# Performance work log

Hardware: AMD Instinct MI355X
Metric: run time of the kernel (lower is better)

The kernel has to match this reference:

```python
import jax, jax.numpy as jnp
import numpy as np

B, N, D, H = 2, 2048, 512, 8
HD = D // H
EPS = 1e-5


def layernorm(x, g, b):
    m = jnp.mean(x, axis=-1, keepdims=True)
    v = jnp.var(x, axis=-1, keepdims=True)
    return (x - m) * jax.lax.rsqrt(v + EPS) * g + b


def setup_inputs() -> dict:
    key = jax.random.key(0)
    ks = jax.random.split(key, 16)
    s = 1.0 / np.sqrt(D)
    def lin(k, din, dout):
        k1, k2 = jax.random.split(k)
        return (jax.random.uniform(k1, (din, dout), jnp.float32, -s, s),
                jax.random.uniform(k2, (dout,), jnp.float32, -s, s))
    Wq, bq = lin(ks[0], D, D)
    Wk, bk = lin(ks[1], D, D)
    Wv, bv = lin(ks[2], D, D)
    Wo, bo = lin(ks[3], D, D)
    W1, b1 = lin(ks[4], D, 2 * D)
    W2, b2 = lin(ks[5], 2 * D, D)
    return {
        'y': jax.random.normal(ks[6], (B, N, D), jnp.float32),
        'Wq': Wq, 'bq': bq, 'Wk': Wk, 'bk': bk, 'Wv': Wv, 'bv': bv,
        'Wo': Wo, 'bo': bo,
        'ln1_g': jnp.ones((D,)), 'ln1_b': jnp.zeros((D,)),
        'ln2_g': jnp.ones((D,)), 'ln2_b': jnp.zeros((D,)),
        'W1': W1, 'b1': b1, 'W2': W2, 'b2': b2,
    }


def reference(y, Wq, bq, Wk, bk, Wv, bv, Wo, bo, ln1_g, ln1_b, ln2_g, ln2_b, W1, b1, W2, b2):
    x = layernorm(y, ln1_g, ln1_b)
    def heads(W, b):
        return (x @ W + b).reshape(B, N, H, HD).transpose(0, 2, 1, 3)  # bhnc
    q = heads(Wq, bq)
    k = heads(Wk, bk)
    v = heads(Wv, bv)
    score = jax.nn.softmax(jnp.einsum('bhic,bhjc->bhij', q, k) / np.sqrt(HD), axis=-1)
    r = jnp.einsum('bhij,bhjc->bhic', score, v)
    r = r.transpose(0, 2, 1, 3).reshape(B, N, D) @ Wo + bo
    y = y + r
    h = layernorm(y, ln2_g, ln2_b)
    h = jax.nn.gelu(h @ W1 + b1, approximate=False) @ W2 + b2
    return y + h
```

## Files before the change

### kernel.cpp

```cpp
#include <hip/hip_runtime.h>

#define DEVI __device__ __forceinline__

typedef unsigned short u16;
typedef unsigned int   u32;
typedef unsigned long long u64;
typedef float  f32x4  __attribute__((ext_vector_type(4)));
typedef __bf16 bf16x8 __attribute__((ext_vector_type(8)));

union FragU { bf16x8 b; u64 u[2]; __bf16 e[8]; };

DEVI u16 f2b(float x) { __bf16 t = (__bf16)x; return __builtin_bit_cast(u16, t); }

DEVI float exp2a(float x) { float r; asm("v_exp_f32 %0, %1" : "=v"(r) : "v"(x)); return r; }

DEVI void gload16(const void* g, void* l) {
  __builtin_amdgcn_global_load_lds((const __attribute__((address_space(1))) u32*)g,
                                   (__attribute__((address_space(3))) u32*)l, 16, 0, 0);
}

DEVI int kperm(int b) {
  return (b & 0x47) | ((b & 0x18) << 1) | ((b & 0x20) >> 2);
}
DEVI int swzo(int row, int b) {
  const int p = kperm(b);
  return ((((p >> 4) ^ row) & 7) << 4) | (p & 15);
}
DEVI FragU ldfrag(const char* base, int row, int g) {
  return *reinterpret_cast<const FragU*>(base + row * 128 + (((g ^ (row & 7)) << 4)));
}
DEVI size_t gaddr(int row, int kbyte, int rowbytes) {
  return (size_t)row * rowbytes + (size_t)((kbyte & ~127) + swzo(row, kbyte & 127));
}

__global__ __launch_bounds__(256)
void prep(const float* __restrict__ Wq, const float* __restrict__ Wk,
          const float* __restrict__ Wv, const float* __restrict__ Wo,
          const float* __restrict__ W1, const float* __restrict__ W2,
          u16* __restrict__ wqkvT, u16* __restrict__ woT,
          u16* __restrict__ w1T, u16* __restrict__ w2T,
          const float* __restrict__ y, const float* __restrict__ ln1g,
          const float* __restrict__ ln1b, char* __restrict__ xb) {
  const int id = blockIdx.x;
  if (id < 2048) {
    __shared__ float tile[32][33];
    const float* src; u16* dst; int K, N, bx, by;
    if (id < 1024) {
      const int m = id >> 8, t = id & 255;
      K = 512; N = 512; bx = t & 15; by = t >> 4;
      src = (m == 0) ? Wq : (m == 1) ? Wk : (m == 2) ? Wv : Wo;
      dst = (m == 3) ? woT : wqkvT + m * 512 * 512;
    } else if (id < 1536) {
      const int t = id - 1024; K = 512; N = 1024; bx = t & 31; by = t >> 5;
      src = W1; dst = w1T;
    } else {
      const int t = id - 1536; K = 1024; N = 512; bx = t & 15; by = t >> 4;
      src = W2; dst = w2T;
    }
    const int tx = threadIdx.x & 31, ty = threadIdx.x >> 5;
#pragma unroll
    for (int i = 0; i < 4; ++i)
      tile[ty + i * 8][tx] = src[(size_t)(by * 32 + ty + i * 8) * N + bx * 32 + tx];
    __syncthreads();
    const int nl = threadIdx.x >> 3, kq = threadIdx.x & 7;
    const int n = bx * 32 + nl;
    const int kg = by * 32 + kq * 4;
    union { ushort4 s; u64 q; } pk;
    pk.s.x = f2b(tile[kq * 4 + 0][nl]);
    pk.s.y = f2b(tile[kq * 4 + 1][nl]);
    pk.s.z = f2b(tile[kq * 4 + 2][nl]);
    pk.s.w = f2b(tile[kq * 4 + 3][nl]);
    *(u64*)((char*)dst + gaddr(n, 2 * kg, 2 * K)) = pk.q;
  } else {
    const int row = id - 2048;
    const int t = threadIdx.x;
    const float2 v = ((const float2*)(y + (size_t)row * 512))[t];
    float s1 = v.x + v.y, s2 = v.x * v.x + v.y * v.y;
#pragma unroll
    for (int off = 32; off; off >>= 1) { s1 += __shfl_xor(s1, off); s2 += __shfl_xor(s2, off); }
    __shared__ float a1[4], a2[4];
    const int w = t >> 6;
    if ((t & 63) == 0) { a1[w] = s1; a2[w] = s2; }
    __syncthreads();
    s1 = a1[0] + a1[1] + a1[2] + a1[3];
    s2 = a2[0] + a2[1] + a2[2] + a2[3];
    const float mean = s1 * (1.f / 512.f);
    const float var = s2 * (1.f / 512.f) - mean * mean;
    const float rstd = rsqrtf(var + 1e-5f);
    const float2 gg = ((const float2*)ln1g)[t];
    const float2 bb = ((const float2*)ln1b)[t];
    const u16 o0 = f2b((v.x - mean) * rstd * gg.x + bb.x);
    const u16 o1 = f2b((v.y - mean) * rstd * gg.y + bb.y);
    *(u32*)(xb + gaddr(row, 4 * t, 1024)) = (u32)o0 | ((u32)o1 << 16);
  }
}

__global__ __launch_bounds__(256)
void ln_bf16(const float* __restrict__ x, const float* __restrict__ g,
             const float* __restrict__ b, char* __restrict__ out) {
  const int row = blockIdx.x;
  const int t = threadIdx.x;
  const float2 v = ((const float2*)(x + (size_t)row * 512))[t];
  float s1 = v.x + v.y, s2 = v.x * v.x + v.y * v.y;
#pragma unroll
  for (int off = 32; off; off >>= 1) { s1 += __shfl_xor(s1, off); s2 += __shfl_xor(s2, off); }
  __shared__ float a1[4], a2[4];
  const int w = t >> 6;
  if ((t & 63) == 0) { a1[w] = s1; a2[w] = s2; }
  __syncthreads();
  s1 = a1[0] + a1[1] + a1[2] + a1[3];
  s2 = a2[0] + a2[1] + a2[2] + a2[3];
  const float mean = s1 * (1.f / 512.f);
  const float var = s2 * (1.f / 512.f) - mean * mean;
  const float rstd = rsqrtf(var + 1e-5f);
  const float2 gg = ((const float2*)g)[t];
  const float2 bb = ((const float2*)b)[t];
  const u16 o0 = f2b((v.x - mean) * rstd * gg.x + bb.x);
  const u16 o1 = f2b((v.y - mean) * rstd * gg.y + bb.y);
  *(u32*)(out + gaddr(row, 4 * t, 1024)) = (u32)o0 | ((u32)o1 << 16);
}

enum { EPI_QKV = 0, EPI_RES = 1, EPI_GELU = 2 };

template <int EPI, int WM, int WN, int AM, int AN>
__global__ __launch_bounds__(WM * WN * 64)
void gemm_bf16(const char* __restrict__ A, const char* __restrict__ Bt, int N, int K,
               const float* __restrict__ bias,
               const float* __restrict__ bq, const float* __restrict__ bk,
               const float* __restrict__ bv,
               const float* __restrict__ res, float* __restrict__ outF,
               char* __restrict__ outB,
               u16* __restrict__ qo, char* __restrict__ ko, char* __restrict__ vo) {
  constexpr int NW = WM * WN;
  constexpr int TM = WM * AM * 16, TN = WN * AN * 16;
  constexpr int NCHA = TM / 8, NCHB = TN / 8, NCH = NCHA + NCHB;
  constexpr int CPW = NCH / NW;
  static_assert(CPW * NW == NCH, "chunk split");
  __shared__ __align__(16) char sA[2][TM * 128];
  __shared__ __align__(16) char sB[2][TN * 128];
  const int tid = threadIdx.x;
  const int l = tid & 63, w = tid >> 6;
  const int tm = blockIdx.x, tn = blockIdx.y;
  const int wr = w / WN, wc = w % WN;
  const int u = l >> 4, r16 = l & 15;
  const int lrow = l >> 3, lgr = l & 7;
  f32x4 acc[AM][AN] = {};
  const size_t KB = (size_t)K * 2;
  const char* Ab = A + (size_t)(tm * TM) * KB;
  const char* Bb = Bt + (size_t)(tn * TN) * KB;
  const int nkt = K >> 6;
  auto stage = [&](int buf, int kt) {
#pragma unroll
    for (int i = 0; i < CPW; ++i) {
      const int c = w * CPW + i;
      if (c < NCHA) {
        gload16(Ab + (size_t)(c * 8 + lrow) * KB + (size_t)kt * 128 + (lgr << 4),
                sA[buf] + c * 1024);
      } else {
        const int c2 = c - NCHA;
        gload16(Bb + (size_t)(c2 * 8 + lrow) * KB + (size_t)kt * 128 + (lgr << 4),
                sB[buf] + c2 * 1024);
      }
    }
  };
  stage(0, 0);
  int cur = 0;
  for (int kt = 0; kt < nkt; ++kt) {
    __syncthreads();
    if (kt + 1 < nkt) stage(cur ^ 1, kt + 1);
    __builtin_amdgcn_s_setprio(1);
#pragma unroll
    for (int ks = 0; ks < 2; ++ks) {
      FragU af[AM], bfr[AN];
      const int g = ks * 4 + u;
#pragma unroll
      for (int i = 0; i < AM; ++i)
        af[i] = ldfrag(sA[cur], wr * (AM * 16) + i * 16 + r16, g);
#pragma unroll
      for (int i = 0; i < AN; ++i)
        bfr[i] = ldfrag(sB[cur], wc * (AN * 16) + i * 16 + r16, g);
#pragma unroll
      for (int mi = 0; mi < AM; ++mi)
#pragma unroll
        for (int ni = 0; ni < AN; ++ni)
          acc[mi][ni] = __builtin_amdgcn_mfma_f32_16x16x32_bf16(af[mi].b, bfr[ni].b,
                                                                acc[mi][ni], 0, 0, 0);
    }
    __builtin_amdgcn_s_setprio(0);
    cur ^= 1;
  }
  const int row0 = tm * TM + wr * (AM * 16) + (u << 2);
  const int col0 = tn * TN + wc * (AN * 16) + r16;
#pragma unroll
  for (int mi = 0; mi < AM; ++mi) {
#pragma unroll
    for (int ni = 0; ni < AN; ++ni) {
      const int col = col0 + ni * 16;
      if (EPI == EPI_RES) {
#pragma unroll
        for (int r = 0; r < 4; ++r) {
          const int row = row0 + mi * 16 + r;
          outF[(size_t)row * N + col] = acc[mi][ni][r] + bias[col] + res[(size_t)row * N + col];
        }
      } else if (EPI == EPI_GELU) {
#pragma unroll
        for (int r = 0; r < 4; ++r) {
          const int row = row0 + mi * 16 + r;
          const float x = acc[mi][ni][r] + bias[col];
          *(u16*)(outB + gaddr(row, 2 * col, 2 * N)) =
              f2b(0.5f * x * (1.f + erff(x * 0.70710678118f)));
        }
      } else {
        const int which = col >> 9, cc = col & 511;
        const int h = cc >> 6, hd = cc & 63;
        if (which == 2) {
          const int rowa = row0 + mi * 16;
          const int bb2 = rowa >> 11, nt0 = rowa & 2047;
          const int bh = bb2 * 8 + h;
          const float bvv = bv[cc];
          union { ushort4 s; u64 q; } pk;
          pk.s.x = f2b(acc[mi][ni][0] + bvv);
          pk.s.y = f2b(acc[mi][ni][1] + bvv);
          pk.s.z = f2b(acc[mi][ni][2] + bvv);
          pk.s.w = f2b(acc[mi][ni][3] + bvv);
          *(u64*)(vo + (size_t)bh * 262144 + (size_t)(nt0 >> 6) * 8192 +
                  gaddr(hd, 2 * (nt0 & 63), 128)) = pk.q;
        } else {
#pragma unroll
          for (int r = 0; r < 4; ++r) {
            const int row = row0 + mi * 16 + r;
            const int bb2 = row >> 11, nt = row & 2047;
            const int bh = bb2 * 8 + h;
            if (which == 0)
              qo[((size_t)bh * 2048 + nt) * 64 + hd] = f2b((acc[mi][ni][r] + bq[cc]) * 0.18033688f);
            else
              *(u16*)(ko + (size_t)bh * 262144 + (size_t)(nt >> 6) * 8192 +
                      gaddr(nt & 63, 2 * hd, 128)) = f2b(acc[mi][ni][r] + bk[cc]);
          }
        }
      }
    }
  }
}

__global__ __launch_bounds__(512)
void attn_k(const u16* __restrict__ q, const char* __restrict__ kswz,
            const char* __restrict__ vswz, char* __restrict__ r_out) {
  __shared__ __align__(16) char sK[2][2][8192];
  __shared__ __align__(16) char sV[2][2][8192];
  const int tid = threadIdx.x;
  const int l = tid & 63, w = tid >> 6;
  const int kvh = w & 1, qw = w >> 1;
  const int bh = blockIdx.x, qt = blockIdx.y;
  const int u = l >> 4, r16 = l & 15;
  const char* kp = kswz + (size_t)bh * 262144;
  const char* vp = vswz + (size_t)bh * 262144;
  const int c0 = qw * 2;
  auto stage = [&](int buf, int t) {
#pragma unroll
    for (int c = 0; c < 2; ++c) {
      gload16(kp + (size_t)t * 8192 + (c0 + c) * 1024 + l * 16, sK[kvh][buf] + (c0 + c) * 1024);
      gload16(vp + (size_t)t * 8192 + (c0 + c) * 1024 + l * 16, sV[kvh][buf] + (c0 + c) * 1024);
    }
  };
  stage(0, kvh * 16);
  FragU qf[2], ones;
  {
    const u16* qr = q + (size_t)bh * (2048 * 64) + (size_t)(qt * 64 + qw * 16 + r16) * 64 + (u << 2);
    qf[0].u[0] = *(const u64*)qr;        qf[0].u[1] = *(const u64*)(qr + 16);
    qf[1].u[0] = *(const u64*)(qr + 32); qf[1].u[1] = *(const u64*)(qr + 48);
    ones.u[0] = 0x3F803F803F803F80ull;
    ones.u[1] = 0x3F803F803F803F80ull;
  }
  f32x4 o[4] = {};
  f32x4 lacc = {};
  int cur = 0;
  for (int i = 0; i < 16; ++i) {
    __syncthreads();
    if (i < 15) stage(cur ^ 1, kvh * 16 + i + 1);
    f32x4 st[4] = {};
    __builtin_amdgcn_s_setprio(1);
#pragma unroll
    for (int ks = 0; ks < 2; ++ks) {
      const int g = ks * 4 + u;
#pragma unroll
      for (int mi = 0; mi < 4; ++mi) {
        const FragU kf = ldfrag(sK[kvh][cur], mi * 16 + r16, g);
        st[mi] = __builtin_amdgcn_mfma_f32_16x16x32_bf16(kf.b, qf[ks].b, st[mi], 0, 0, 0);
      }
    }
    __builtin_amdgcn_s_setprio(0);
#pragma unroll
    for (int mi = 0; mi < 4; ++mi)
#pragma unroll
      for (int r = 0; r < 4; ++r) st[mi][r] = exp2a(st[mi][r]);
    FragU pb[2];
#pragma unroll
    for (int ks = 0; ks < 2; ++ks)
#pragma unroll
      for (int j = 0; j < 4; ++j) {
        pb[ks].e[j]     = (__bf16)st[2 * ks][j];
        pb[ks].e[j + 4] = (__bf16)st[2 * ks + 1][j];
      }
    __builtin_amdgcn_s_setprio(1);
#pragma unroll
    for (int ks = 0; ks < 2; ++ks) {
      const int g = ks * 4 + u;
      lacc = __builtin_amdgcn_mfma_f32_16x16x32_bf16(ones.b, pb[ks].b, lacc, 0, 0, 0);
#pragma unroll
      for (int mo = 0; mo < 4; ++mo) {
        const FragU vf = ldfrag(sV[kvh][cur], mo * 16 + r16, g);
        o[mo] = __builtin_amdgcn_mfma_f32_16x16x32_bf16(vf.b, pb[ks].b, o[mo], 0, 0, 0);
      }
    }
    __builtin_amdgcn_s_setprio(0);
    cur ^= 1;
  }
  __syncthreads();
  float* scrO = (float*)&sK[0][0][0];
  float* scrL = (float*)&sV[0][0][0];
  if (kvh == 1) {
    if (u == 0) scrL[qw * 32 + r16] = lacc[0];
#pragma unroll
    for (int mo = 0; mo < 4; ++mo)
#pragma unroll
      for (int r = 0; r < 4; ++r)
        scrO[qw * 1024 + (mo * 16 + u * 4 + r) * 16 + r16] = o[mo][r];
  }
  __syncthreads();
  if (kvh == 0) {
    const float linv = 1.f / (lacc[0] + scrL[qw * 32 + r16]);
    const int tok = (bh >> 3) * 2048 + qt * 64 + qw * 16 + r16;
    const int h = bh & 7;
#pragma unroll
    for (int mo = 0; mo < 4; ++mo) {
      union { ushort4 s; u64 qq; } pk;
      float vv[4];
#pragma unroll
      for (int r = 0; r < 4; ++r)
        vv[r] = (o[mo][r] + scrO[qw * 1024 + (mo * 16 + u * 4 + r) * 16 + r16]) * linv;
      pk.s.x = f2b(vv[0]); pk.s.y = f2b(vv[1]); pk.s.z = f2b(vv[2]); pk.s.w = f2b(vv[3]);
      *(u64*)(r_out + (size_t)tok * 1024 + h * 128 + swzo(tok, mo * 32 + (u << 3))) = pk.qq;
    }
  }
}

extern "C" void kernel_launch(void* const* d_in, const int* in_sizes, int n_in,
                              void* d_out, int out_size, void* d_ws, size_t ws_size,
                              hipStream_t stream) {
  const float* y    = (const float*)d_in[0];
  const float* Wq   = (const float*)d_in[1];
  const float* bq   = (const float*)d_in[2];
  const float* Wk   = (const float*)d_in[3];
  const float* bk   = (const float*)d_in[4];
  const float* Wv   = (const float*)d_in[5];
  const float* bv   = (const float*)d_in[6];
  const float* Wo   = (const float*)d_in[7];
  const float* bo   = (const float*)d_in[8];
  const float* ln1g = (const float*)d_in[9];
  const float* ln1b = (const float*)d_in[10];
  const float* ln2g = (const float*)d_in[11];
  const float* ln2b = (const float*)d_in[12];
  const float* W1   = (const float*)d_in[13];
  const float* b1   = (const float*)d_in[14];
  const float* W2   = (const float*)d_in[15];
  const float* b2   = (const float*)d_in[16];
  float* out = (float*)d_out;
  char* ws = (char*)d_ws;
  char* xb    = ws;
  u16*  qb    = (u16*)(ws + (4u << 20));
  char* kswz  = ws + (8u << 20);
  char* vswz  = ws + (12u << 20);
  char* rb    = ws + (16u << 20);
  char* g1b   = ws + (20u << 20);
  u16* wqkvT  = (u16*)(ws + (28u << 20));
  u16* woT    = wqkvT + 1536 * 512;
  u16* w1T    = woT + 512 * 512;
  u16* w2T    = w1T + 1024 * 512;

  prep<<<6144, 256, 0, stream>>>(Wq, Wk, Wv, Wo, W1, W2, wqkvT, woT, w1T, w2T,
                                 y, ln1g, ln1b, xb);
  gemm_bf16<EPI_QKV, 2, 2, 4, 2><<<dim3(32, 24), 256, 0, stream>>>(
      xb, (const char*)wqkvT, 1536, 512, nullptr, bq, bk, bv,
      nullptr, nullptr, nullptr, qb, kswz, vswz);
  attn_k<<<dim3(16, 32), 512, 0, stream>>>(qb, kswz, vswz, rb);
  gemm_bf16<EPI_RES, 2, 2, 2, 2><<<dim3(64, 8), 256, 0, stream>>>(
      rb, (const char*)woT, 512, 512, bo, nullptr, nullptr, nullptr,
      y, out, nullptr, nullptr, nullptr, nullptr);
  ln_bf16<<<4096, 256, 0, stream>>>(out, ln2g, ln2b, xb);
  gemm_bf16<EPI_GELU, 2, 2, 4, 2><<<dim3(32, 16), 256, 0, stream>>>(
      xb, (const char*)w1T, 1024, 512, b1, nullptr, nullptr, nullptr,
      nullptr, nullptr, g1b, nullptr, nullptr, nullptr);
  gemm_bf16<EPI_RES, 2, 2, 2, 2><<<dim3(64, 8), 256, 0, stream>>>(
      g1b, (const char*)w2T, 512, 1024, b2, nullptr, nullptr, nullptr,
      out, out, nullptr, nullptr, nullptr, nullptr);
}
```

Measured before the change: 91.47 us.

## Halve attention block to 4 waves with two query tiles per wave; widen GELU GEMM tile

Each attention block now runs 4 waves instead of 8, and each wave handles 32 query rows (two 16-row fragments). This reuses every K and V LDS fragment load across two MFMAs, and each wave stages twice as many K/V chunks. The cost is more accumulator registers per wave and half as many resident waves to hide latency. Separately, the FFN1 GEMM tile is widened along N, halving its grid, which cuts B-operand reloads but lowers parallelism.

```diff
diff --git a/kernel.cpp b/kernel.cpp
--- a/kernel.cpp
+++ b/kernel.cpp
@@ -243,7 +243,7 @@
   }
 }
 
-__global__ __launch_bounds__(512)
+__global__ __launch_bounds__(256)
 void attn_k(const u16* __restrict__ q, const char* __restrict__ kswz,
             const char* __restrict__ vswz, char* __restrict__ r_out) {
   __shared__ __align__(16) char sK[2][2][8192];
@@ -255,30 +255,35 @@
   const int u = l >> 4, r16 = l & 15;
   const char* kp = kswz + (size_t)bh * 262144;
   const char* vp = vswz + (size_t)bh * 262144;
-  const int c0 = qw * 2;
   auto stage = [&](int buf, int t) {
 #pragma unroll
-    for (int c = 0; c < 2; ++c) {
-      gload16(kp + (size_t)t * 8192 + (c0 + c) * 1024 + l * 16, sK[kvh][buf] + (c0 + c) * 1024);
-      gload16(vp + (size_t)t * 8192 + (c0 + c) * 1024 + l * 16, sV[kvh][buf] + (c0 + c) * 1024);
+    for (int c = 0; c < 4; ++c) {
+      gload16(kp + (size_t)t * 8192 + qw * 4096 + c * 1024 + l * 16,
+              sK[kvh][buf] + qw * 4096 + c * 1024);
+      gload16(vp + (size_t)t * 8192 + qw * 4096 + c * 1024 + l * 16,
+              sV[kvh][buf] + qw * 4096 + c * 1024);
     }
   };
   stage(0, kvh * 16);
-  FragU qf[2], ones;
+  FragU qf[2][2], ones;
   {
-    const u16* qr = q + (size_t)bh * (2048 * 64) + (size_t)(qt * 64 + qw * 16 + r16) * 64 + (u << 2);
-    qf[0].u[0] = *(const u64*)qr;        qf[0].u[1] = *(const u64*)(qr + 16);
-    qf[1].u[0] = *(const u64*)(qr + 32); qf[1].u[1] = *(const u64*)(qr + 48);
+#pragma unroll
+    for (int f = 0; f < 2; ++f) {
+      const u16* qr = q + (size_t)bh * (2048 * 64) +
+                      (size_t)(qt * 64 + qw * 32 + f * 16 + r16) * 64 + (u << 2);
+      qf[f][0].u[0] = *(const u64*)qr;        qf[f][0].u[1] = *(const u64*)(qr + 16);
+      qf[f][1].u[0] = *(const u64*)(qr + 32); qf[f][1].u[1] = *(const u64*)(qr + 48);
+    }
     ones.u[0] = 0x3F803F803F803F80ull;
     ones.u[1] = 0x3F803F803F803F80ull;
   }
-  f32x4 o[4] = {};
-  f32x4 lacc = {};
+  f32x4 o[4][2] = {};
+  f32x4 lacc[2] = {};
   int cur = 0;
   for (int i = 0; i < 16; ++i) {
     __syncthreads();
     if (i < 15) stage(cur ^ 1, kvh * 16 + i + 1);
-    f32x4 st[4] = {};
+    f32x4 st[4][2] = {};
     __builtin_amdgcn_s_setprio(1);
 #pragma unroll
     for (int ks = 0; ks < 2; ++ks) {
@@ -286,31 +291,43 @@
 #pragma unroll
       for (int mi = 0; mi < 4; ++mi) {
         const FragU kf = ldfrag(sK[kvh][cur], mi * 16 + r16, g);
-        st[mi] = __builtin_amdgcn_mfma_f32_16x16x32_bf16(kf.b, qf[ks].b, st[mi], 0, 0, 0);
+#pragma unroll
+        for (int f = 0; f < 2; ++f)
+          st[mi][f] = __builtin_amdgcn_mfma_f32_16x16x32_bf16(kf.b, qf[f][ks].b,
+                                                              st[mi][f], 0, 0, 0);
       }
     }
     __builtin_amdgcn_s_setprio(0);
 #pragma unroll
     for (int mi = 0; mi < 4; ++mi)
 #pragma unroll
-      for (int r = 0; r < 4; ++r) st[mi][r] = exp2a(st[mi][r]);
-    FragU pb[2];
-#pragma unroll
-    for (int ks = 0; ks < 2; ++ks)
-#pragma unroll
-      for (int j = 0; j < 4; ++j) {
-        pb[ks].e[j]     = (__bf16)st[2 * ks][j];
-        pb[ks].e[j + 4] = (__bf16)st[2 * ks + 1][j];
-      }
+      for (int f = 0; f < 2; ++f)
+#pragma unroll
+        for (int r = 0; r < 4; ++r) st[mi][f][r] = exp2a(st[mi][f][r]);
+    FragU pb[2][2];
+#pragma unroll
+    for (int f = 0; f < 2; ++f)
+#pragma unroll
+      for (int ks = 0; ks < 2; ++ks)
+#pragma unroll
+        for (int j = 0; j < 4; ++j) {
+          pb[f][ks].e[j]     = (__bf16)st[2 * ks][f][j];
+          pb[f][ks].e[j + 4] = (__bf16)st[2 * ks + 1][f][j];
+        }
     __builtin_amdgcn_s_setprio(1);
 #pragma unroll
     for (int ks = 0; ks < 2; ++ks) {
       const int g = ks * 4 + u;
-      lacc = __builtin_amdgcn_mfma_f32_16x16x32_bf16(ones.b, pb[ks].b, lacc, 0, 0, 0);
+#pragma unroll
+      for (int f = 0; f < 2; ++f)
+        lacc[f] = __builtin_amdgcn_mfma_f32_16x16x32_bf16(ones.b, pb[f][ks].b, lacc[f], 0, 0, 0);
 #pragma unroll
       for (int mo = 0; mo < 4; ++mo) {
         const FragU vf = ldfrag(sV[kvh][cur], mo * 16 + r16, g);
-        o[mo] = __builtin_amdgcn_mfma_f32_16x16x32_bf16(vf.b, pb[ks].b, o[mo], 0, 0, 0);
+#pragma unroll
+        for (int f = 0; f < 2; ++f)
+          o[mo][f] = __builtin_amdgcn_mfma_f32_16x16x32_bf16(vf.b, pb[f][ks].b,
+                                                             o[mo][f], 0, 0, 0);
       }
     }
     __builtin_amdgcn_s_setprio(0);
@@ -320,27 +337,34 @@
   float* scrO = (float*)&sK[0][0][0];
   float* scrL = (float*)&sV[0][0][0];
   if (kvh == 1) {
-    if (u == 0) scrL[qw * 32 + r16] = lacc[0];
+    if (u == 0)
+#pragma unroll
+      for (int f = 0; f < 2; ++f) scrL[qw * 32 + f * 16 + r16] = lacc[f][0];
 #pragma unroll
     for (int mo = 0; mo < 4; ++mo)
 #pragma unroll
-      for (int r = 0; r < 4; ++r)
-        scrO[qw * 1024 + (mo * 16 + u * 4 + r) * 16 + r16] = o[mo][r];
+      for (int f = 0; f < 2; ++f)
+#pragma unroll
+        for (int r = 0; r < 4; ++r)
+          scrO[qw * 2048 + (mo * 16 + u * 4 + r) * 32 + f * 16 + r16] = o[mo][f][r];
   }
   __syncthreads();
   if (kvh == 0) {
-    const float linv = 1.f / (lacc[0] + scrL[qw * 32 + r16]);
-    const int tok = (bh >> 3) * 2048 + qt * 64 + qw * 16 + r16;
     const int h = bh & 7;
 #pragma unroll
-    for (int mo = 0; mo < 4; ++mo) {
-      union { ushort4 s; u64 qq; } pk;
-      float vv[4];
-#pragma unroll
-      for (int r = 0; r < 4; ++r)
-        vv[r] = (o[mo][r] + scrO[qw * 1024 + (mo * 16 + u * 4 + r) * 16 + r16]) * linv;
-      pk.s.x = f2b(vv[0]); pk.s.y = f2b(vv[1]); pk.s.z = f2b(vv[2]); pk.s.w = f2b(vv[3]);
-      *(u64*)(r_out + (size_t)tok * 1024 + h * 128 + swzo(tok, mo * 32 + (u << 3))) = pk.qq;
+    for (int f = 0; f < 2; ++f) {
+      const float linv = 1.f / (lacc[f][0] + scrL[qw * 32 + f * 16 + r16]);
+      const int tok = (bh >> 3) * 2048 + qt * 64 + qw * 32 + f * 16 + r16;
+#pragma unroll
+      for (int mo = 0; mo < 4; ++mo) {
+        union { ushort4 s; u64 qq; } pk;
+        float vv[4];
+#pragma unroll
+        for (int r = 0; r < 4; ++r)
+          vv[r] = (o[mo][f][r] + scrO[qw * 2048 + (mo * 16 + u * 4 + r) * 32 + f * 16 + r16]) * linv;
+        pk.s.x = f2b(vv[0]); pk.s.y = f2b(vv[1]); pk.s.z = f2b(vv[2]); pk.s.w = f2b(vv[3]);
+        *(u64*)(r_out + (size_t)tok * 1024 + h * 128 + swzo(tok, mo * 32 + (u << 3))) = pk.qq;
+      }
     }
   }
 }
@@ -383,12 +407,12 @@
   gemm_bf16<EPI_QKV, 2, 2, 4, 2><<<dim3(32, 24), 256, 0, stream>>>(
       xb, (const char*)wqkvT, 1536, 512, nullptr, bq, bk, bv,
       nullptr, nullptr, nullptr, qb, kswz, vswz);
-  attn_k<<<dim3(16, 32), 512, 0, stream>>>(qb, kswz, vswz, rb);
+  attn_k<<<dim3(16, 32), 256, 0, stream>>>(qb, kswz, vswz, rb);
   gemm_bf16<EPI_RES, 2, 2, 2, 2><<<dim3(64, 8), 256, 0, stream>>>(
       rb, (const char*)woT, 512, 512, bo, nullptr, nullptr, nullptr,
       y, out, nullptr, nullptr, nullptr, nullptr);
   ln_bf16<<<4096, 256, 0, stream>>>(out, ln2g, ln2b, xb);
-  gemm_bf16<EPI_GELU, 2, 2, 4, 2><<<dim3(32, 16), 256, 0, stream>>>(
+  gemm_bf16<EPI_GELU, 2, 2, 4, 4><<<dim3(32, 8), 256, 0, stream>>>(
       xb, (const char*)w1T, 1024, 512, b1, nullptr, nullptr, nullptr,
       nullptr, nullptr, g1b, nullptr, nullptr, nullptr);
   gemm_bf16<EPI_RES, 2, 2, 2, 2><<<dim3(64, 8), 256, 0, stream>>>(
```

New measurement: 98.40 us. +7.6%, slower.
